# Performance work log

Measured on AMD Instinct MI355X. Metric: run time of the kernel, lower is better.

Reference implementation:

```python
import jax, jax.numpy as jnp
import numpy as np

D_MODEL = 1024; D_STATE = 64; HEADDIM = 64; EXPAND = 2
D_INNER = EXPAND * D_MODEL            # 2048
NHEADS = D_INNER // HEADDIM           # 32
NGROUPS = 1
GN = NGROUPS * D_STATE                # 64
CONV_DIM = D_INNER + 2 * (2 * GN)     # 2304
D_IN_PROJ = 2 * D_INNER + 2 * (2 * GN) + 2 * NHEADS  # 4416
K_SP = 7; K_TP = 4; CHUNK = 256
BATCH = 2; FRAMES = 8; SPATIAL = 256; SEQLEN = SPATIAL * FRAMES  # 2048


def silu(x):
    return x * jax.nn.sigmoid(x)


def flip_frames(x, f):
    # 'b (l f) d -> b l f d' flip frame axis, flatten back
    b, L, d = x.shape
    return x.reshape(b, L // f, f, d)[:, :, ::-1, :].reshape(b, L, d)


def depthwise_conv1d(x, w, b, pad):
    # x: (N, L, C), w: (C, K) depthwise, pad=(lo,hi) -> (N, L_out, C)
    y = jax.lax.conv_general_dilated(
        jnp.transpose(x, (0, 2, 1)), w[:, None, :], (1,), [pad],
        feature_group_count=w.shape[0])
    return jnp.transpose(y + b[None, :, None], (0, 2, 1))


def setup_inputs():
    rng = np.random.default_rng(0)
    f32 = lambda *s: jnp.asarray(rng.standard_normal(s), jnp.float32)
    # dt_bias init exactly as in the torch module
    dt = np.exp(rng.random(NHEADS) * (np.log(0.1) - np.log(0.001)) + np.log(0.001))
    dt = np.clip(dt, 1e-4, None)
    inv_dt = dt + np.log(-np.expm1(-dt))
    return {
        "u": f32(BATCH, SEQLEN, D_MODEL),
        "in_proj_w": f32(D_IN_PROJ, D_MODEL) * 0.02,
        "conv_sp_w": f32(CONV_DIM, K_SP) * 0.2,
        "conv_sp_b": f32(CONV_DIM) * 0.02,
        "conv_tp_w": f32(CONV_DIM, K_TP) * 0.2,
        "conv_tp_b": f32(CONV_DIM) * 0.02,
        "dt_bias": jnp.asarray(inv_dt, jnp.float32),
        "A_log": jnp.zeros((NHEADS,), jnp.float32),
        "D": jnp.ones((NHEADS,), jnp.float32),
        "fc_D_w": f32(NHEADS, D_INNER) * 0.02,
        "norm_w": jnp.ones((D_INNER,), jnp.float32),
        "out_proj_w": f32(D_MODEL, D_INNER) * 0.02,
        "num_frames": FRAMES,
    }


def chunked_scan(xh, dt, A, Bm, Cm, sp, cs):
    # xh:(R,L,h,p) dt:(R,L,h) Bm,Cm:(R,L,n). ngroups=1.
    # seq_idx semantics: rows [0:b) one segment; rows [b:2b) reset every sp tokens.
    R, L, H, P = xh.shape
    nch = L // cs
    b = R // 2
    xch = xh.reshape(R, nch, cs, H, P)
    dtc = jnp.transpose(dt.reshape(R, nch, cs, H), (0, 1, 3, 2))   # (R,nch,h,cs)
    Bch = Bm.reshape(R, nch, cs, D_STATE)
    Cch = Cm.reshape(R, nch, cs, D_STATE)
    a = dtc * A[None, None, :, None]                               # negative logs
    cum = jnp.cumsum(a, axis=-1)                                   # inclusive
    mask = jnp.tril(jnp.ones((cs, cs), bool))
    seg = cum[..., :, None] - cum[..., None, :]                    # (R,nch,h,t,s)
    Lmat = jnp.where(mask, jnp.exp(jnp.where(mask, seg, 0.0)), 0.0)
    CB = jnp.einsum('rctn,rcsn->rcts', Cch, Bch)
    M = CB[:, :, None] * Lmat * dtc[:, :, :, None, :]
    Y_intra = jnp.einsum('rchts,rcshp->rcthp', M, xch)
    # chunk-final states and cross-chunk recurrence
    G = jnp.exp(cum[..., -1:] - cum) * dtc                         # (R,nch,h,cs)
    S_chunk = jnp.einsum('rchs,rcshp,rcsn->rchpn', G, xch, Bch)
    chunk_decay = jnp.exp(cum[..., -1])                            # (R,nch,h)
    cidx = jnp.arange(nch)
    rb = (cidx > 0) & ((cidx * cs) % sp == 0)
    resetc = jnp.concatenate([jnp.zeros((b, nch), bool),
                              jnp.broadcast_to(rb, (b, nch))], axis=0)

    def cstep(S, inp):
        dec, Sc, r = inp
        S = jnp.where(r[:, None, None, None], 0.0, S)
        prev = S
        S = dec[:, :, None, None] * S + Sc
        return S, prev

    S0 = jnp.zeros((R, H, P, D_STATE), xh.dtype)
    _, prevs = jax.lax.scan(
        cstep, S0,
        (jnp.transpose(chunk_decay, (1, 0, 2)),
         jnp.transpose(S_chunk, (1, 0, 2, 3, 4)),
         resetc.T))
    prev_states = jnp.transpose(prevs, (1, 0, 2, 3, 4))            # (R,nch,h,p,n)
    Y_inter = jnp.einsum('rcht,rctn,rchpn->rcthp', jnp.exp(cum), Cch, prev_states)
    return (Y_intra + Y_inter).reshape(R, L, H, P)


def reference(u, in_proj_w, conv_sp_w, conv_sp_b, conv_tp_w, conv_tp_b,
              dt_bias, A_log, D, fc_D_w, norm_w, out_proj_w, num_frames):
    batch, seqlen, _ = u.shape
    f = num_frames
    sp = seqlen // f
    zxbcdt = u @ in_proj_w.T
    z = zxbcdt[..., :D_INNER]
    xBC = zxbcdt[..., D_INNER:D_INNER + CONV_DIM]
    dt_raw = zxbcdt[..., D_INNER + CONV_DIM:]
    dt = jnp.concatenate([dt_raw[..., :NHEADS],
                          flip_frames(dt_raw[..., NHEADS:], f)], axis=0)
    dt = jax.nn.softplus(dt + dt_bias)                             # (2b,L,h)
    A = -jnp.exp(A_log)
    # spatial depthwise conv over spatial dim per frame ('same' pad) + SiLU
    xBC = xBC.reshape(batch, sp, f, CONV_DIM).transpose(0, 2, 1, 3).reshape(batch * f, sp, CONV_DIM)
    xBC = silu(depthwise_conv1d(xBC, conv_sp_w, conv_sp_b, (K_SP // 2, K_SP // 2)))
    # causal temporal depthwise conv over frame dim per spatial location + SiLU
    xBC = xBC.reshape(batch, f, sp, CONV_DIM).transpose(0, 2, 1, 3).reshape(batch * sp, f, CONV_DIM)
    xBC = silu(depthwise_conv1d(xBC, conv_tp_w, conv_tp_b, (K_TP - 1, 0)))
    xBC = xBC.reshape(batch, seqlen, CONV_DIM)
    x = xBC[..., :D_INNER]
    BC = xBC[..., D_INNER:]
    x_orig = x
    x2 = jnp.concatenate([x, flip_frames(x, f)], axis=0)
    BC2 = jnp.concatenate([BC[..., :2 * GN], flip_frames(BC[..., 2 * GN:], f)], axis=0)
    Bm, Cm = BC2[..., :GN], BC2[..., GN:]
    xh = x2.reshape(2 * batch, seqlen, NHEADS, HEADDIM)
    y = chunked_scan(xh, dt, A, Bm, Cm, sp, CHUNK)                 # (2b,L,h,p)
    y_fwd = y[:batch].reshape(batch, seqlen, D_INNER)
    y_rev = y[batch:].reshape(batch, sp, f, D_INNER)
    # roll-by-one with zeroed first position (fwd: token axis, rev: spatial axis)
    y_fwd = jnp.concatenate([jnp.zeros_like(y_fwd[:, :1]), y_fwd[:, :-1]], axis=1)
    y_rev = jnp.concatenate([jnp.zeros_like(y_rev[:, :1]), y_rev[:, :-1]], axis=1)
    y_rev = y_rev[:, :, ::-1, :].reshape(batch, seqlen, D_INNER)
    x_res = x_orig * jnp.repeat(x_orig @ fc_D_w.T + D, HEADDIM, axis=-1)
    y = y_fwd + y_rev + x_res
    # gated RMSNorm (norm_before_gate=True): rmsnorm(y)*w*silu(z)
    y = y * jax.lax.rsqrt(jnp.mean(jnp.square(y), axis=-1, keepdims=True) + 1e-5)
    y = y * norm_w * silu(z)
    return y @ out_proj_w.T
```

## Files before the change

### kernel.cpp

```cpp
#include <hip/hip_runtime.h>
#include <hip/hip_bf16.h>
#include <math.h>

#define D_STATE   64
#define HEADDIM   64
#define D_INNER   2048
#define NHEADS    32
#define GN        64
#define CONV_DIM  2304
#define D_IN_PROJ 4416
#define ZLD       4352
#define K_SP      7
#define K_TP      4
#define CHUNK     256
#define BATCHN    2
#define FRAMES    8
#define SPATIAL   256
#define SEQLEN    2048
#define NCH       8
#define MTOT      4096

typedef __attribute__((ext_vector_type(8))) short short8;
typedef __attribute__((ext_vector_type(8))) unsigned short ushort8v;
typedef __attribute__((ext_vector_type(4))) float floatx4;

__device__ __forceinline__ float silu_f(float x) { return x / (1.f + __expf(-x)); }
__device__ __forceinline__ int flip_l(int l) { return (l & ~7) | (7 - (l & 7)); }
__device__ __forceinline__ unsigned short f2bf(float f) {
  unsigned int u = __float_as_uint(f);
  unsigned int r = (u + 0x7fffu + ((u >> 16) & 1u)) >> 16;
  return (unsigned short)r;
}
__device__ __forceinline__ float bf2f(unsigned short s) {
  return __uint_as_float(((unsigned int)s) << 16);
}
__device__ __forceinline__ unsigned int cvtpk_bf16(float lo, float hi) {
  unsigned int r;
  asm("v_cvt_pk_bf16_f32 %0, %1, %2" : "=v"(r) : "v"(lo), "v"(hi));
  return r;
}
typedef union { short8 v; unsigned int u[4]; } s8u;
__device__ __forceinline__ void gload_lds16(const unsigned short* g, unsigned short* l) {
  __builtin_amdgcn_global_load_lds((const __attribute__((address_space(1))) void*)g,
                                   (__attribute__((address_space(3))) void*)l, 16, 0, 0);
}

__global__ __launch_bounds__(256) void cast3_bf16_kernel(const float* __restrict__ a,
                                                         unsigned short* __restrict__ oa,
                                                         int na,
                                                         const float* __restrict__ b,
                                                         unsigned short* __restrict__ ob,
                                                         int nb,
                                                         const float* __restrict__ c,
                                                         unsigned short* __restrict__ oc) {
  int bid = blockIdx.x;
  const float* in;
  unsigned short* out;
  size_t blk;
  if (bid < na)            { in = a; out = oa; blk = bid; }
  else if (bid < na + nb)  { in = b; out = ob; blk = bid - na; }
  else                     { in = c; out = oc; blk = bid - na - nb; }
  size_t i = (blk * 256 + threadIdx.x) * 4;
  float4 v = *(const float4*)(in + i);
  ushort4 o;
  o.x = f2bf(v.x); o.y = f2bf(v.y); o.z = f2bf(v.z); o.w = f2bf(v.w);
  *(ushort4*)(out + i) = o;
}

__global__ __launch_bounds__(256) void gemm_bk64_bf16out(
    const unsigned short* __restrict__ A, int lda,
    const unsigned short* __restrict__ B, int ldb,
    unsigned short* __restrict__ C, int ldc, int K) {
  __shared__ unsigned short As[128 * 64];
  __shared__ unsigned short Bs[128 * 64];
  const int tid = threadIdx.x;
  const int lane = tid & 63;
  const int w = tid >> 6;
  const int m0 = blockIdx.y * 128;
  const int n0 = blockIdx.x * 128;
  const int wm = (w >> 1) * 64;
  const int wn = (w & 1) * 64;
  const int lrow = lane >> 3;
  const int lperm = lane & 7;
  floatx4 acc[4][4] = {};
  for (int k0 = 0; k0 < K; k0 += 64) {
#pragma unroll
    for (int j = 0; j < 8; ++j) {
      int g = j * 4 + w;
      if (g < 16) {
        int row = g * 8 + lrow;
        int cg = (lperm ^ (row & 7)) * 8;
        gload_lds16(A + (size_t)(m0 + row) * lda + k0 + cg, &As[g * 512]);
      } else {
        int gb = g - 16;
        int row = gb * 8 + lrow;
        int cg = (lperm ^ (row & 7)) * 8;
        gload_lds16(B + (size_t)(n0 + row) * ldb + k0 + cg, &Bs[gb * 512]);
      }
    }
    __syncthreads();
    const int fr = lane & 15;
    const int kq = (lane >> 4) * 8;
#pragma unroll
    for (int kk = 0; kk < 64; kk += 32) {
      int u = (kk + kq) >> 3;
      short8 af[4], bfr[4];
#pragma unroll
      for (int i = 0; i < 4; ++i) {
        int row = wm + i * 16 + fr;
        af[i] = *(const short8*)&As[(row * 8 + (u ^ (row & 7))) * 8];
      }
#pragma unroll
      for (int j = 0; j < 4; ++j) {
        int row = wn + j * 16 + fr;
        bfr[j] = *(const short8*)&Bs[(row * 8 + (u ^ (row & 7))) * 8];
      }
#pragma unroll
      for (int i = 0; i < 4; ++i)
#pragma unroll
        for (int j = 0; j < 4; ++j)
          acc[i][j] = __builtin_amdgcn_mfma_f32_16x16x32_bf16(af[i], bfr[j], acc[i][j], 0, 0, 0);
    }
    __syncthreads();
  }
  const int fr = lane & 15;
  const int rg = (lane >> 4) * 4;
  unsigned short* Ew = &As[w * 1024];
  const int rr = lane >> 3;
  const int c8 = (lane & 7) * 8;
#pragma unroll
  for (int i = 0; i < 4; ++i) {
#pragma unroll
    for (int q = 0; q < 4; ++q)
#pragma unroll
      for (int j = 0; j < 4; ++j)
        Ew[(rg + q) * 64 + j * 16 + fr] = f2bf(acc[i][j][q]);
    ushort8v v0 = *(const ushort8v*)&Ew[rr * 64 + c8];
    ushort8v v1 = *(const ushort8v*)&Ew[(rr + 8) * 64 + c8];
    *(ushort8v*)(C + (size_t)(m0 + wm + i * 16 + rr) * ldc + n0 + wn + c8) = v0;
    *(ushort8v*)(C + (size_t)(m0 + wm + i * 16 + rr + 8) * ldc + n0 + wn + c8) = v1;
  }
}

__global__ __launch_bounds__(256) void gemm_m64_f32(
    const unsigned short* __restrict__ A, int lda,
    const unsigned short* __restrict__ B, int ldb,
    float* __restrict__ C, int ldc, int K) {
  __shared__ unsigned short As[64 * 64];
  __shared__ unsigned short Bs[128 * 64];
  const int tid = threadIdx.x;
  const int lane = tid & 63;
  const int w = tid >> 6;
  const int m0 = blockIdx.y * 64;
  const int n0 = blockIdx.x * 128;
  const int wm = (w >> 1) * 32;
  const int wn = (w & 1) * 64;
  const int lrow = lane >> 3;
  const int lperm = lane & 7;
  floatx4 acc[2][4] = {};
  for (int k0 = 0; k0 < K; k0 += 64) {
#pragma unroll
    for (int j = 0; j < 6; ++j) {
      int g = j * 4 + w;
      if (g < 8) {
        int row = g * 8 + lrow;
        int cg = (lperm ^ (row & 7)) * 8;
        gload_lds16(A + (size_t)(m0 + row) * lda + k0 + cg, &As[g * 512]);
      } else {
        int gb = g - 8;
        int row = gb * 8 + lrow;
        int cg = (lperm ^ (row & 7)) * 8;
        gload_lds16(B + (size_t)(n0 + row) * ldb + k0 + cg, &Bs[gb * 512]);
      }
    }
    __syncthreads();
    const int fr = lane & 15;
    const int kq = (lane >> 4) * 8;
#pragma unroll
    for (int kk = 0; kk < 64; kk += 32) {
      int u = (kk + kq) >> 3;
      short8 af[2], bfr[4];
#pragma unroll
      for (int i = 0; i < 2; ++i) {
        int row = wm + i * 16 + fr;
        af[i] = *(const short8*)&As[(row * 8 + (u ^ (row & 7))) * 8];
      }
#pragma unroll
      for (int j = 0; j < 4; ++j) {
        int row = wn + j * 16 + fr;
        bfr[j] = *(const short8*)&Bs[(row * 8 + (u ^ (row & 7))) * 8];
      }
#pragma unroll
      for (int i = 0; i < 2; ++i)
#pragma unroll
        for (int j = 0; j < 4; ++j)
          acc[i][j] = __builtin_amdgcn_mfma_f32_16x16x32_bf16(af[i], bfr[j], acc[i][j], 0, 0, 0);
    }
    __syncthreads();
  }
  const int col = lane & 15;
  const int rg = (lane >> 4) * 4;
#pragma unroll
  for (int i = 0; i < 2; ++i)
#pragma unroll
    for (int j = 0; j < 4; ++j)
#pragma unroll
      for (int r = 0; r < 4; ++r)
        C[(size_t)(m0 + wm + i * 16 + rg + r) * ldc + (n0 + wn + j * 16 + col)] = acc[i][j][r];
}

__global__ __launch_bounds__(256) void gemm_ts_mfma(
    const unsigned short* __restrict__ A, int lda,
    const float* __restrict__ B, int ldb,
    float* __restrict__ C, int ldc, int N, int K) {
  __shared__ float red[4][1024];
  const int tid = threadIdx.x;
  const int lane = tid & 63;
  const int w = tid >> 6;
  const int m0 = blockIdx.x * 16;
  const int fr = lane & 15;
  const int kq = (lane >> 4) * 8;
  const int nt = N >> 4;
  const int kseg = K >> 2;
  const int k0 = w * kseg;
  floatx4 acc[4] = {};
  for (int k = k0; k < k0 + kseg; k += 32) {
    short8 af = *(const short8*)(A + (size_t)(m0 + fr) * lda + k + kq);
    for (int j = 0; j < nt; ++j) {
      const float* bp = B + (size_t)(j * 16 + fr) * ldb + k + kq;
      float4 b0 = *(const float4*)bp;
      float4 b1 = *(const float4*)(bp + 4);
      short8 bf8;
      bf8[0] = (short)f2bf(b0.x); bf8[1] = (short)f2bf(b0.y);
      bf8[2] = (short)f2bf(b0.z); bf8[3] = (short)f2bf(b0.w);
      bf8[4] = (short)f2bf(b1.x); bf8[5] = (short)f2bf(b1.y);
      bf8[6] = (short)f2bf(b1.z); bf8[7] = (short)f2bf(b1.w);
      acc[j] = __builtin_amdgcn_mfma_f32_16x16x32_bf16(af, bf8, acc[j], 0, 0, 0);
    }
  }
  const int rg = (lane >> 4) * 4;
  for (int j = 0; j < nt; ++j)
#pragma unroll
    for (int q = 0; q < 4; ++q)
      red[w][j * 256 + (rg + q) * 16 + fr] = acc[j][q];
  __syncthreads();
  const int entries = nt * 256;
  for (int e = tid; e < entries; e += 256) {
    float s = red[0][e] + red[1][e] + red[2][e] + red[3][e];
    int j = e >> 8, idx = e & 255, row = idx >> 4, col = idx & 15;
    C[(size_t)(m0 + row) * ldc + j * 16 + col] = s;
  }
}

__global__ __launch_bounds__(256) void dtscan_kernel(const float* __restrict__ DTraw,
                                                     const float* __restrict__ dt_bias,
                                                     const float* __restrict__ A_log,
                                                     float* __restrict__ DTt,
                                                     float* __restrict__ CUMS) {
  __shared__ float sc[256];
  int tid = threadIdx.x;
  int idx = blockIdx.x * 256 + tid;
  int l  = idx & 2047;
  int rh = idx >> 11;
  int h  = rh & 31;
  int r  = rh >> 5;
  int bi = r & 1;
  int ls = (r < 2) ? l : flip_l(l);
  int ch = (r < 2) ? h : NHEADS + h;
  float raw = DTraw[((size_t)bi * SEQLEN + ls) * 64 + ch] + dt_bias[h];
  float dtv = (raw > 20.f) ? raw : log1pf(__expf(raw));
  DTt[idx] = dtv;
  float A = -__expf(A_log[h]);
  float run = dtv * A;
  sc[tid] = run;
  __syncthreads();
#pragma unroll
  for (int ofs = 1; ofs < 256; ofs <<= 1) {
    float add = (tid >= ofs) ? sc[tid - ofs] : 0.f;
    __syncthreads();
    run += add;
    sc[tid] = run;
    __syncthreads();
  }
  CUMS[idx] = run;
}

__global__ __launch_bounds__(256) void conv_fused2_kernel(const unsigned short* __restrict__ Zb,
                                                          const float* __restrict__ wsp,
                                                          const float* __restrict__ bsp,
                                                          const float* __restrict__ wtp,
                                                          const float* __restrict__ btp,
                                                          unsigned short* __restrict__ XTb) {
  __shared__ float4 xsl[8][8][32];
  const int tid = threadIdx.x;
  const int g  = tid & 31;
  const int fr = tid >> 5;
  const int c  = blockIdx.x * 128 + g * 4;
  const int s0 = blockIdx.y * 8;
  const int bi = blockIdx.z;
  float wsp_r[4][K_SP];
#pragma unroll
  for (int ch = 0; ch < 4; ++ch)
#pragma unroll
    for (int j = 0; j < K_SP; ++j) wsp_r[ch][j] = wsp[(c + ch) * K_SP + j];
  float4 bsp4 = *(const float4*)(bsp + c);
  float4 z[14];
#pragma unroll
  for (int i = 0; i < 14; ++i) {
    int ss = s0 - 3 + i;
    if (0 <= ss && ss < SPATIAL) {
      ushort4 v = *(const ushort4*)(Zb + ((size_t)bi * SEQLEN + (ss*8 + fr)) * ZLD + D_INNER + c);
      z[i] = make_float4(bf2f(v.x), bf2f(v.y), bf2f(v.z), bf2f(v.w));
    } else {
      z[i] = make_float4(0.f, 0.f, 0.f, 0.f);
    }
  }
#pragma unroll
  for (int so = 0; so < 8; ++so) {
    float4 a = bsp4;
#pragma unroll
    for (int j = 0; j < K_SP; ++j) {
      a.x += wsp_r[0][j] * z[so + j].x;
      a.y += wsp_r[1][j] * z[so + j].y;
      a.z += wsp_r[2][j] * z[so + j].z;
      a.w += wsp_r[3][j] * z[so + j].w;
    }
    a.x = silu_f(a.x); a.y = silu_f(a.y); a.z = silu_f(a.z); a.w = silu_f(a.w);
    xsl[fr][so][g] = a;
  }
  __syncthreads();
  float wtp_r[4][K_TP];
#pragma unroll
  for (int ch = 0; ch < 4; ++ch)
#pragma unroll
    for (int j = 0; j < K_TP; ++j) wtp_r[ch][j] = wtp[(c + ch) * K_TP + j];
  float4 btp4 = *(const float4*)(btp + c);
#pragma unroll
  for (int so = 0; so < 8; ++so) {
    float4 t = btp4;
#pragma unroll
    for (int j = 0; j < K_TP; ++j) {
      int ff = fr + j - (K_TP - 1);
      if (ff >= 0) {
        float4 xv = xsl[ff][so][g];
        t.x += wtp_r[0][j] * xv.x;
        t.y += wtp_r[1][j] * xv.y;
        t.z += wtp_r[2][j] * xv.z;
        t.w += wtp_r[3][j] * xv.w;
      }
    }
    ushort4 o;
    o.x = f2bf(silu_f(t.x)); o.y = f2bf(silu_f(t.y));
    o.z = f2bf(silu_f(t.z)); o.w = f2bf(silu_f(t.w));
    *(ushort4*)(XTb + ((size_t)bi * SEQLEN + ((s0 + so)*8 + fr)) * CONV_DIM + c) = o;
  }
}

__global__ __launch_bounds__(256) void cb_kernel(const unsigned short* __restrict__ XTb,
                                                 float* __restrict__ CBs) {
  __shared__ float Ct[64][65];
  __shared__ float Bt[64][65];
  int tid = threadIdx.x;
  int t0 = (blockIdx.x & 3) * 64;
  int s0 = (blockIdx.x >> 2) * 64;
  if (s0 > t0) return;
  int c = blockIdx.y;
  int r = blockIdx.z;
  int bi = r & 1;
  int bOff = D_INNER + ((r < 2) ? 0 : 2*GN);
  int cOff = bOff + GN;
  int lrow = tid >> 4;
  int n4 = (tid & 15) << 2;
#pragma unroll
  for (int rep = 0; rep < 4; ++rep) {
    int tl = rep * 16 + lrow;
    int Lc = c * CHUNK + t0 + tl;
    int Ls = c * CHUNK + s0 + tl;
    if (r >= 2) { Lc = flip_l(Lc); Ls = flip_l(Ls); }
    ushort4 cv = *(const ushort4*)(XTb + ((size_t)bi*SEQLEN + Lc)*CONV_DIM + cOff + n4);
    ushort4 bv = *(const ushort4*)(XTb + ((size_t)bi*SEQLEN + Ls)*CONV_DIM + bOff + n4);
    Ct[n4+0][tl] = bf2f(cv.x); Ct[n4+1][tl] = bf2f(cv.y);
    Ct[n4+2][tl] = bf2f(cv.z); Ct[n4+3][tl] = bf2f(cv.w);
    Bt[n4+0][tl] = bf2f(bv.x); Bt[n4+1][tl] = bf2f(bv.y);
    Bt[n4+2][tl] = bf2f(bv.z); Bt[n4+3][tl] = bf2f(bv.w);
  }
  __syncthreads();
  int txx = tid & 15;
  int tyy = tid >> 4;
  float acc[4][4] = {{0.f,0.f,0.f,0.f},{0.f,0.f,0.f,0.f},{0.f,0.f,0.f,0.f},{0.f,0.f,0.f,0.f}};
#pragma unroll
  for (int n = 0; n < D_STATE; ++n) {
    float cr[4], br[4];
#pragma unroll
    for (int i = 0; i < 4; ++i) cr[i] = Ct[n][tyy + 16*i];
#pragma unroll
    for (int j = 0; j < 4; ++j) br[j] = Bt[n][txx + 16*j];
#pragma unroll
    for (int i = 0; i < 4; ++i)
#pragma unroll
      for (int j = 0; j < 4; ++j)
        acc[i][j] += cr[i] * br[j];
  }
  size_t base = (((size_t)r*NCH + c) * CHUNK) * CHUNK;
#pragma unroll
  for (int i = 0; i < 4; ++i)
#pragma unroll
    for (int j = 0; j < 4; ++j)
      CBs[base + (size_t)(t0 + tyy + 16*i)*CHUNK + (s0 + txx + 16*j)] = acc[i][j];
}

__global__ __launch_bounds__(256) void chunk_state_kernel(const unsigned short* __restrict__ XTb,
                                                          const float* __restrict__ DTt,
                                                          const float* __restrict__ CUMS,
                                                          float* __restrict__ SCH) {
  __shared__ unsigned short Xs[64 * 136];
  __shared__ unsigned short Bs[64 * 136];
  __shared__ float gs[CHUNK];
  int tid = threadIdx.x;
  int lane = tid & 63;
  int w = tid >> 6;
  int c = blockIdx.x;
  int h = blockIdx.y;
  int r = blockIdx.z;
  int bi = r;
  int rh = r * NHEADS + h;
  float cl = CUMS[(size_t)rh*SEQLEN + c*CHUNK + 255];
  gs[tid] = __expf(cl - CUMS[(size_t)rh*SEQLEN + c*CHUNK + tid]) * DTt[(size_t)rh*SEQLEN + c*CHUNK + tid];
  const int fr = lane & 15;
  const int kq = (lane >> 4) * 8;
  const int sr = tid >> 3;
  const int p0 = (tid & 7) * 8;
  const int swz = (tid & 7) << 3;
  floatx4 acc[4] = {};
  for (int half = 0; half < 2; ++half) {
    __syncthreads();
#pragma unroll
    for (int P = 0; P < 4; ++P) {
      int s = P * 32 + sr;
      int l = c*CHUNK + half*128 + s;
      const unsigned short* row = XTb + ((size_t)bi*SEQLEN + l)*CONV_DIM;
      ushort8v xv = *(const ushort8v*)(row + h*HEADDIM + p0);
      ushort8v bv = *(const ushort8v*)(row + D_INNER + p0);
      float g = gs[half*128 + s];
      int cswz = s ^ swz;
#pragma unroll
      for (int q = 0; q < 8; ++q) {
        Xs[(p0 + q) * 136 + cswz] = f2bf(g * bf2f(xv[q]));
        Bs[(p0 + q) * 136 + cswz] = bv[q];
      }
    }
    __syncthreads();
#pragma unroll
    for (int sl = 0; sl < 4; ++sl) {
      int s0 = sl * 32;
      int Ra = w*16 + fr;
      short8 af = *(const short8*)&Xs[Ra * 136 + ((s0 + kq) ^ (((Ra >> 3) & 7) << 3))];
#pragma unroll
      for (int j = 0; j < 4; ++j) {
        int Rb = j*16 + fr;
        short8 bf8 = *(const short8*)&Bs[Rb * 136 + ((s0 + kq) ^ (((Rb >> 3) & 7) << 3))];
        acc[j] = __builtin_amdgcn_mfma_f32_16x16x32_bf16(af, bf8, acc[j], 0, 0, 0);
      }
    }
  }
  const int col = lane & 15;
  const int rg = (lane >> 4) * 4;
  size_t base = (((size_t)r*NCH + c)*NHEADS + h) * (size_t)(HEADDIM*D_STATE);
#pragma unroll
  for (int j = 0; j < 4; ++j)
#pragma unroll
    for (int q = 0; q < 4; ++q)
      SCH[base + (size_t)(w*16 + rg + q)*D_STATE + j*16 + col] = acc[j][q];
}

__global__ __launch_bounds__(256) void state_combine_kernel(const float* __restrict__ SCH,
                                                            const float* __restrict__ CUMS,
                                                            float* __restrict__ SPREV) {
  int bid = blockIdx.x;
  int pq = bid & 3;
  int h = (bid >> 2) & 31;
  int r = bid >> 7;
  int tid = threadIdx.x;
  int p = pq*16 + (tid >> 4);
  int n = (tid & 15) * 4;
  float4 S = make_float4(0.f, 0.f, 0.f, 0.f);
  for (int c = 0; c < NCH; ++c) {
    size_t off = ((((size_t)r*NCH + c)*NHEADS + h)*HEADDIM + p)*D_STATE + n;
    *(float4*)(SPREV + off) = S;
    float dec = __expf(CUMS[((size_t)r*NHEADS + h)*SEQLEN + c*CHUNK + 255]);
    float4 v = *(const float4*)(SCH + off);
    S.x = dec*S.x + v.x; S.y = dec*S.y + v.y;
    S.z = dec*S.z + v.z; S.w = dec*S.w + v.w;
  }
}

#define YS_ED(S0)                                                              \
  float edv[8];                                                                \
  { float4 e0_ = *(const float4*)&ecd[(S0) + kq];                              \
    float4 e1_ = *(const float4*)&ecd[(S0) + kq + 4];                          \
    edv[0]=e0_.x; edv[1]=e0_.y; edv[2]=e0_.z; edv[3]=e0_.w;                    \
    edv[4]=e1_.x; edv[5]=e1_.y; edv[6]=e1_.z; edv[7]=e1_.w; }

#define YS_BFR(S0)                                                             \
  short8 bfr[4];                                                               \
  _Pragma("unroll")                                                            \
  for (int j = 0; j < 4; ++j) {                                                \
    int R = j * 16 + fr;                                                       \
    bfr[j] = *(const short8*)&Xt[R * 264 + (((S0) + kq) ^ (((R >> 3) & 7) << 3))]; \
  }

#define YS_MFMA4(AF, ACCROW)                                                   \
  _Pragma("unroll")                                                            \
  for (int j = 0; j < 4; ++j)                                                  \
    ACCROW[j] = __builtin_amdgcn_mfma_f32_16x16x32_bf16(AF, bfr[j], ACCROW[j], 0, 0, 0);

#define YS_AF_NOMASK(C0, C1, E)                                                \
  { af_.u[0] = cvtpk_bf16(C0.x*(E)*edv[0], C0.y*(E)*edv[1]);                   \
    af_.u[1] = cvtpk_bf16(C0.z*(E)*edv[2], C0.w*(E)*edv[3]);                   \
    af_.u[2] = cvtpk_bf16(C1.x*(E)*edv[4], C1.y*(E)*edv[5]);                   \
    af_.u[3] = cvtpk_bf16(C1.z*(E)*edv[6], C1.w*(E)*edv[7]); }

#define YS_AF_MASK(C0, C1, E, TROW)                                            \
  { float wz[8] = {C0.x,C0.y,C0.z,C0.w,C1.x,C1.y,C1.z,C1.w};                   \
    _Pragma("unroll")                                                          \
    for (int jj = 0; jj < 8; ++jj) {                                           \
      float t_ = wz[jj]*(E)*edv[jj];                                           \
      wz[jj] = (kq + jj <= (TROW)) ? t_ : 0.f; }                               \
    af_.u[0]=cvtpk_bf16(wz[0],wz[1]); af_.u[1]=cvtpk_bf16(wz[2],wz[3]);        \
    af_.u[2]=cvtpk_bf16(wz[4],wz[5]); af_.u[3]=cvtpk_bf16(wz[6],wz[7]); }

#define YS_STRIP(KS, E2, ACC)                                                  \
  {                                                                            \
    const int t0s_ = (KS) * 32;                                                \
    const float* cbr0 = CBs + cbbase + (size_t)(t0s_ + fr) * CHUNK + kq;       \
    const float* cbr1 = cbr0 + (size_t)16 * CHUNK;                             \
    float4 a0 = *(const float4*)cbr0;                                          \
    float4 a1 = *(const float4*)(cbr0 + 4);                                    \
    float4 b0 = *(const float4*)cbr1;                                          \
    float4 b1 = *(const float4*)(cbr1 + 4);                                    \
    for (int sl = 0; sl < (KS); ++sl) {                                        \
      int s0 = sl * 32;                                                        \
      float4 na0 = *(const float4*)(cbr0 + s0 + 32);                           \
      float4 na1 = *(const float4*)(cbr0 + s0 + 36);                           \
      float4 nb0 = *(const float4*)(cbr1 + s0 + 32);                           \
      float4 nb1 = *(const float4*)(cbr1 + s0 + 36);                           \
      YS_ED(s0); YS_BFR(s0);                                                   \
      s8u af_;                                                                 \
      YS_AF_NOMASK(a0, a1, (E2)[0]);                                           \
      YS_MFMA4(af_.v, ACC[0]);                                                 \
      YS_AF_NOMASK(b0, b1, (E2)[1]);                                           \
      YS_MFMA4(af_.v, ACC[1]);                                                 \
      a0 = na0; a1 = na1; b0 = nb0; b1 = nb1;                                  \
    }                                                                          \
    {                                                                          \
      int s0 = (KS) * 32;                                                      \
      YS_ED(s0); YS_BFR(s0);                                                   \
      s8u af_;                                                                 \
      YS_AF_MASK(a0, a1, (E2)[0], fr);                                         \
      YS_MFMA4(af_.v, ACC[0]);                                                 \
      YS_AF_MASK(b0, b1, (E2)[1], 16 + fr);                                    \
      YS_MFMA4(af_.v, ACC[1]);                                                 \
    }                                                                          \
  }

#define YS_INTER(T0S, E2, ACC)                                                 \
  _Pragma("unroll")                                                            \
  for (int i = 0; i < 2; ++i) {                                                \
    int t = (T0S) + i * 16 + fr;                                               \
    const unsigned short* crow = XTb + ((size_t)bi*SEQLEN + c*CHUNK + t)*CONV_DIM + D_INNER + GN + n0 + kq; \
    ushort4 c0 = *(const ushort4*)crow;                                        \
    ushort4 c1 = *(const ushort4*)(crow + 4);                                  \
    float eI = (E2)[i];                                                        \
    s8u af_;                                                                   \
    af_.u[0] = cvtpk_bf16(bf2f(c0.x)*eI, bf2f(c0.y)*eI);                       \
    af_.u[1] = cvtpk_bf16(bf2f(c0.z)*eI, bf2f(c0.w)*eI);                       \
    af_.u[2] = cvtpk_bf16(bf2f(c1.x)*eI, bf2f(c1.y)*eI);                       \
    af_.u[3] = cvtpk_bf16(bf2f(c1.z)*eI, bf2f(c1.w)*eI);                       \
    YS_MFMA4(af_.v, ACC[i]);                                                   \
  }

#define YS_EPI(T0S, ACC)                                                       \
  _Pragma("unroll")                                                            \
  for (int i = 0; i < 2; ++i) {                                                \
    _Pragma("unroll")                                                          \
    for (int q = 0; q < 4; ++q)                                                \
      _Pragma("unroll")                                                        \
      for (int j = 0; j < 4; ++j)                                              \
        Ew[(rg + q) * 64 + j * 16 + fr] = f2bf(ACC[i][j][q]);                  \
    ushort8v v0 = *(const ushort8v*)&Ew[rr * 64 + c8];                         \
    ushort8v v1 = *(const ushort8v*)&Ew[(rr + 8) * 64 + c8];                   \
    *(ushort8v*)(Yb16 + ybase + (size_t)((T0S) + i*16 + rr) * D_INNER + c8) = v0;      \
    *(ushort8v*)(Yb16 + ybase + (size_t)((T0S) + i*16 + rr + 8) * D_INNER + c8) = v1;  \
  }

__global__ __launch_bounds__(256, 4) void yscan_kernel(const unsigned short* __restrict__ XTb,
                                                       const float* __restrict__ DTt,
                                                       const float* __restrict__ CUMS,
                                                       const float* __restrict__ CBs,
                                                       const float* __restrict__ SPREV,
                                                       unsigned short* __restrict__ Yb16) {
  __shared__ unsigned short Xt[64 * 264];
  __shared__ float cums[CHUNK];
  __shared__ float ecd[CHUNK];
  int tid = threadIdx.x;
  int lane = tid & 63;
  int w = tid >> 6;
  int id = blockIdx.x;
  int c = id & 7;
  int h = (id >> 3) & 31;
  int r = id >> 8;
  int rh = r * NHEADS + h;
  int bi = r & 1;
  {
    int sr = tid >> 3;
    int p0 = (tid & 7) * 8;
    int swz = (tid & 7) << 3;
#pragma unroll
    for (int P = 0; P < 8; ++P) {
      int s = P * 32 + sr;
      int L = c * CHUNK + s;
      if (r >= 2) L = flip_l(L);
      ushort8v v = *(const ushort8v*)(XTb + ((size_t)bi * SEQLEN + L) * CONV_DIM + h * HEADDIM + p0);
      int cswz = s ^ swz;
#pragma unroll
      for (int q = 0; q < 8; ++q)
        Xt[(p0 + q) * 264 + cswz] = v[q];
    }
    float cv = CUMS[(size_t)rh * SEQLEN + c * CHUNK + tid];
    cums[tid] = cv;
    ecd[tid] = __expf(-cv) * DTt[(size_t)rh * SEQLEN + c * CHUNK + tid];
  }
  __syncthreads();
  const int fr = lane & 15;
  const int kq = (lane >> 4) * 8;
  const int kA = w, kB = 7 - w;
  const int tA = kA * 32, tB = kB * 32;
  float eAr[2], eBr[2];
#pragma unroll
  for (int i = 0; i < 2; ++i) {
    eAr[i] = __expf(cums[tA + i * 16 + fr]);
    eBr[i] = __expf(cums[tB + i * 16 + fr]);
  }
  floatx4 accA[2][4] = {};
  floatx4 accB[2][4] = {};
  size_t cbbase = (((size_t)r * NCH + c) * CHUNK) * CHUNK;
  YS_STRIP(kA, eAr, accA);
  YS_STRIP(kB, eBr, accB);
  if (r < 2) {
    const float* spbase = SPREV + (((size_t)r*NCH + c)*NHEADS + h) * (size_t)(HEADDIM*D_STATE);
#pragma unroll
    for (int ns = 0; ns < 2; ++ns) {
      int n0 = ns * 32;
      short8 bfr[4];
#pragma unroll
      for (int j = 0; j < 4; ++j) {
        const float* sp = spbase + (size_t)(j*16 + fr)*D_STATE + n0 + kq;
        float4 s0v = *(const float4*)sp;
        float4 s1v = *(const float4*)(sp + 4);
        s8u bb;
        bb.u[0] = cvtpk_bf16(s0v.x, s0v.y);
        bb.u[1] = cvtpk_bf16(s0v.z, s0v.w);
        bb.u[2] = cvtpk_bf16(s1v.x, s1v.y);
        bb.u[3] = cvtpk_bf16(s1v.z, s1v.w);
        bfr[j] = bb.v;
      }
      YS_INTER(tA, eAr, accA);
      YS_INTER(tB, eBr, accB);
    }
  }
  __syncthreads();
  unsigned short* Ew = Xt + w * 1024;
  const int rg = (lane >> 4) * 4;
  const int rr = lane >> 3;
  const int c8 = (lane & 7) * 8;
  size_t ybase = ((size_t)r*SEQLEN + c*CHUNK)*D_INNER + h*HEADDIM;
  YS_EPI(tA, accA);
  YS_EPI(tB, accB);
}

__global__ __launch_bounds__(256) void combine_kernel(const unsigned short* __restrict__ Y,
                                                      const unsigned short* __restrict__ XTb,
                                                      const float* __restrict__ FCD,
                                                      const float* __restrict__ Dp,
                                                      const unsigned short* __restrict__ Zb,
                                                      const float* __restrict__ norm_w,
                                                      unsigned short* __restrict__ YPb) {
  __shared__ float red[256];
  int row = blockIdx.x;
  int bi = row >> 11;
  int l = row & 2047;
  int s = l >> 3, fr = l & 7;
  int tid = threadIdx.x;
  int d0 = tid * 8;
  const unsigned short* yf = (l >= 1) ? Y + ((size_t)bi*SEQLEN + (l-1))*D_INNER + d0 : nullptr;
  const unsigned short* yr = (s >= 1) ? Y + ((size_t)(2+bi)*SEQLEN + ((s-1)*8 + (7-fr)))*D_INNER + d0 : nullptr;
  const unsigned short* xr = XTb + ((size_t)row)*CONV_DIM + d0;
  float fcv = FCD[(size_t)row*NHEADS + (d0 >> 6)] + Dp[d0 >> 6];
  ushort8v xv8 = *(const ushort8v*)xr;
  float v[8];
#pragma unroll
  for (int q = 0; q < 8; ++q) v[q] = bf2f(xv8[q]) * fcv;
  if (yf) {
    ushort8v a = *(const ushort8v*)yf;
#pragma unroll
    for (int q = 0; q < 8; ++q) v[q] += bf2f(a[q]);
  }
  if (yr) {
    ushort8v a = *(const ushort8v*)yr;
#pragma unroll
    for (int q = 0; q < 8; ++q) v[q] += bf2f(a[q]);
  }
  float ss = 0.f;
#pragma unroll
  for (int q = 0; q < 8; ++q) ss += v[q] * v[q];
  red[tid] = ss;
  __syncthreads();
  for (int ofs = 128; ofs > 0; ofs >>= 1) {
    if (tid < ofs) red[tid] += red[tid + ofs];
    __syncthreads();
  }
  float rs = rsqrtf(red[0] / (float)D_INNER + 1e-5f);
  ushort8v zv8 = *(const ushort8v*)(Zb + ((size_t)row)*ZLD + d0);
  float4 nw0 = *(const float4*)(norm_w + d0);
  float4 nw1 = *(const float4*)(norm_w + d0 + 4);
  float nw[8] = {nw0.x,nw0.y,nw0.z,nw0.w,nw1.x,nw1.y,nw1.z,nw1.w};
  ushort8v o;
#pragma unroll
  for (int q = 0; q < 8; ++q)
    o[q] = f2bf(v[q] * rs * nw[q] * silu_f(bf2f(zv8[q])));
  *(ushort8v*)(YPb + (size_t)row*D_INNER + d0) = o;
}

extern "C" void kernel_launch(void* const* d_in, const int* in_sizes, int n_in,
                              void* d_out, int out_size, void* d_ws, size_t ws_size,
                              hipStream_t stream) {
  (void)in_sizes; (void)n_in; (void)out_size; (void)ws_size;
  const float* u          = (const float*)d_in[0];
  const float* in_proj_w  = (const float*)d_in[1];
  const float* conv_sp_w  = (const float*)d_in[2];
  const float* conv_sp_b  = (const float*)d_in[3];
  const float* conv_tp_w  = (const float*)d_in[4];
  const float* conv_tp_b  = (const float*)d_in[5];
  const float* dt_bias    = (const float*)d_in[6];
  const float* A_log      = (const float*)d_in[7];
  const float* Dp         = (const float*)d_in[8];
  const float* fc_D_w     = (const float*)d_in[9];
  const float* norm_w     = (const float*)d_in[10];
  const float* out_proj_w = (const float*)d_in[11];
  float* out = (float*)d_out;
  float* ws = (float*)d_ws;

  float* Z     = ws;
  float* SH    = Z     + 17825792ULL;
  float* XT    = SH    + 9437184ULL;
  float* DTt   = XT    + 9437184ULL;
  float* Yb    = DTt   + 262144ULL;
  float* SPREV = Yb    + 16777216ULL;
  float* FCD   = SPREV + 2097152ULL;
  float* DTraw = FCD   + 131072ULL;
  float* CUMS  = DTraw + 262144ULL;

  unsigned short* Zb   = (unsigned short*)Z;
  unsigned short* XTb  = (unsigned short*)XT;
  unsigned short* Yb16 = (unsigned short*)Yb;
  unsigned short* Ub   = (unsigned short*)Yb;
  unsigned short* Wb   = (unsigned short*)Yb + 4194304ULL;
  float* SCH = Yb + 8388608ULL;
  unsigned short* Wob = (unsigned short*)(Yb + 10485760ULL);
  unsigned short* YPb = (unsigned short*)SH;

  cast3_bf16_kernel<<<10496, 256, 0, stream>>>(u, Ub, 4096, in_proj_w, Wb, 4352,
                                               out_proj_w, Wob);
  gemm_bk64_bf16out<<<dim3(34, 32), 256, 0, stream>>>(Ub, 1024, Wb, 1024, Zb, ZLD, 1024);
  gemm_ts_mfma<<<256, 256, 0, stream>>>(Ub, 1024, in_proj_w + 4352ULL*1024, 1024,
                                        DTraw, 64, 64, 1024);
  dtscan_kernel<<<1024, 256, 0, stream>>>(DTraw, dt_bias, A_log, DTt, CUMS);
  conv_fused2_kernel<<<dim3(18, 32, 2), 256, 0, stream>>>(Zb, conv_sp_w, conv_sp_b,
                                                          conv_tp_w, conv_tp_b, XTb);
  gemm_ts_mfma<<<256, 256, 0, stream>>>(XTb, CONV_DIM, fc_D_w, 2048,
                                        FCD, 32, 32, 2048);
  cb_kernel<<<dim3(16, 8, 4), 256, 0, stream>>>(XTb, SH);
  chunk_state_kernel<<<dim3(NCH, NHEADS, 2), 256, 0, stream>>>(XTb, DTt, CUMS, SCH);
  state_combine_kernel<<<256, 256, 0, stream>>>(SCH, CUMS, SPREV);
  yscan_kernel<<<dim3(1024), 256, 0, stream>>>(XTb, DTt, CUMS, SH, SPREV, Yb16);
  combine_kernel<<<4096, 256, 0, stream>>>(Yb16, XTb, FCD, Dp, Zb, norm_w, YPb);
  gemm_m64_f32<<<dim3(8, 64), 256, 0, stream>>>(YPb, 2048, Wob, 2048, out, 1024, 2048);
}
```

Measured before the change: 328.7 us.

## Remap GEMM blocks per XCD, use MFMA in cb_kernel, shuffle-reduce RMS norm

The two GEMMs switch to a 1D grid whose block index is remapped so each XCD (bid&7) handles a contiguous rectangular region of output tiles, improving L2 reuse of A and B tiles. cb_kernel drops its LDS-staged FP32 outer-product loop in favour of bf16 MFMA 16x16x32 instructions that read fragments directly from global memory. combine_kernel replaces its shared-memory tree reduction, which synchronised at every step, with wave shuffles plus a single four-element LDS reduction. The MFMA path accumulates from bf16 inputs in fp32, as the FP32 version already did after converting from bf16, so numerics should stay close.

```diff
diff --git a/kernel.cpp b/kernel.cpp
--- a/kernel.cpp
+++ b/kernel.cpp
@@ -76,8 +76,13 @@
   const int tid = threadIdx.x;
   const int lane = tid & 63;
   const int w = tid >> 6;
-  const int m0 = blockIdx.y * 128;
-  const int n0 = blockIdx.x * 128;
+  const int bid = blockIdx.x;
+  const int xcd = bid & 7;
+  const int rp  = bid >> 3;
+  const int px  = rp % 17;
+  const int py  = rp / 17;
+  const int m0 = ((xcd >> 1) * 8 + py) * 128;
+  const int n0 = ((xcd & 1) * 17 + px) * 128;
   const int wm = (w >> 1) * 64;
   const int wn = (w & 1) * 64;
   const int lrow = lane >> 3;
@@ -151,8 +156,14 @@
   const int tid = threadIdx.x;
   const int lane = tid & 63;
   const int w = tid >> 6;
-  const int m0 = blockIdx.y * 64;
-  const int n0 = blockIdx.x * 128;
+  const int bid = blockIdx.x;
+  const int xcd = bid & 7;
+  const int q8  = bid >> 3;
+  const int rsel = q8 >> 5;
+  const int rp   = q8 & 31;
+  const int reg  = xcd + 8 * rsel;
+  const int m0 = ((reg >> 1) * 8 + (rp >> 2)) * 64;
+  const int n0 = ((reg & 1) * 4 + (rp & 3)) * 128;
   const int wm = (w >> 1) * 32;
   const int wn = (w & 1) * 64;
   const int lrow = lane >> 3;
@@ -358,9 +369,9 @@
 
 __global__ __launch_bounds__(256) void cb_kernel(const unsigned short* __restrict__ XTb,
                                                  float* __restrict__ CBs) {
-  __shared__ float Ct[64][65];
-  __shared__ float Bt[64][65];
   int tid = threadIdx.x;
+  int lane = tid & 63;
+  int w = tid >> 6;
   int t0 = (blockIdx.x & 3) * 64;
   int s0 = (blockIdx.x >> 2) * 64;
   if (s0 > t0) return;
@@ -369,44 +380,32 @@
   int bi = r & 1;
   int bOff = D_INNER + ((r < 2) ? 0 : 2*GN);
   int cOff = bOff + GN;
-  int lrow = tid >> 4;
-  int n4 = (tid & 15) << 2;
-#pragma unroll
-  for (int rep = 0; rep < 4; ++rep) {
-    int tl = rep * 16 + lrow;
-    int Lc = c * CHUNK + t0 + tl;
-    int Ls = c * CHUNK + s0 + tl;
-    if (r >= 2) { Lc = flip_l(Lc); Ls = flip_l(Ls); }
-    ushort4 cv = *(const ushort4*)(XTb + ((size_t)bi*SEQLEN + Lc)*CONV_DIM + cOff + n4);
-    ushort4 bv = *(const ushort4*)(XTb + ((size_t)bi*SEQLEN + Ls)*CONV_DIM + bOff + n4);
-    Ct[n4+0][tl] = bf2f(cv.x); Ct[n4+1][tl] = bf2f(cv.y);
-    Ct[n4+2][tl] = bf2f(cv.z); Ct[n4+3][tl] = bf2f(cv.w);
-    Bt[n4+0][tl] = bf2f(bv.x); Bt[n4+1][tl] = bf2f(bv.y);
-    Bt[n4+2][tl] = bf2f(bv.z); Bt[n4+3][tl] = bf2f(bv.w);
-  }
-  __syncthreads();
-  int txx = tid & 15;
-  int tyy = tid >> 4;
-  float acc[4][4] = {{0.f,0.f,0.f,0.f},{0.f,0.f,0.f,0.f},{0.f,0.f,0.f,0.f},{0.f,0.f,0.f,0.f}};
-#pragma unroll
-  for (int n = 0; n < D_STATE; ++n) {
-    float cr[4], br[4];
-#pragma unroll
-    for (int i = 0; i < 4; ++i) cr[i] = Ct[n][tyy + 16*i];
-#pragma unroll
-    for (int j = 0; j < 4; ++j) br[j] = Bt[n][txx + 16*j];
-#pragma unroll
-    for (int i = 0; i < 4; ++i)
-#pragma unroll
-      for (int j = 0; j < 4; ++j)
-        acc[i][j] += cr[i] * br[j];
-  }
+  const int fr = lane & 15;
+  const int kq = (lane >> 4) * 8;
+  int Lc = c * CHUNK + t0 + w * 16 + fr;
+  if (r >= 2) Lc = flip_l(Lc);
+  const unsigned short* crow = XTb + ((size_t)bi*SEQLEN + Lc)*CONV_DIM + cOff;
+  short8 af0 = *(const short8*)(crow + kq);
+  short8 af1 = *(const short8*)(crow + 32 + kq);
+  floatx4 acc[4] = {};
+#pragma unroll
+  for (int j = 0; j < 4; ++j) {
+    int Ls = c * CHUNK + s0 + j * 16 + fr;
+    if (r >= 2) Ls = flip_l(Ls);
+    const unsigned short* brow = XTb + ((size_t)bi*SEQLEN + Ls)*CONV_DIM + bOff;
+    short8 bf0 = *(const short8*)(brow + kq);
+    short8 bf1 = *(const short8*)(brow + 32 + kq);
+    acc[j] = __builtin_amdgcn_mfma_f32_16x16x32_bf16(af0, bf0, acc[j], 0, 0, 0);
+    acc[j] = __builtin_amdgcn_mfma_f32_16x16x32_bf16(af1, bf1, acc[j], 0, 0, 0);
+  }
+  const int col = lane & 15;
+  const int rg = (lane >> 4) * 4;
   size_t base = (((size_t)r*NCH + c) * CHUNK) * CHUNK;
 #pragma unroll
-  for (int i = 0; i < 4; ++i)
-#pragma unroll
-    for (int j = 0; j < 4; ++j)
-      CBs[base + (size_t)(t0 + tyy + 16*i)*CHUNK + (s0 + txx + 16*j)] = acc[i][j];
+  for (int j = 0; j < 4; ++j)
+#pragma unroll
+    for (int q = 0; q < 4; ++q)
+      CBs[base + (size_t)(t0 + w*16 + rg + q)*CHUNK + (s0 + j*16 + col)] = acc[j][q];
 }
 
 __global__ __launch_bounds__(256) void chunk_state_kernel(const unsigned short* __restrict__ XTb,
@@ -685,7 +684,7 @@
                                                       const unsigned short* __restrict__ Zb,
                                                       const float* __restrict__ norm_w,
                                                       unsigned short* __restrict__ YPb) {
-  __shared__ float red[256];
+  __shared__ float red4[4];
   int row = blockIdx.x;
   int bi = row >> 11;
   int l = row & 2047;
@@ -713,13 +712,12 @@
   float ss = 0.f;
 #pragma unroll
   for (int q = 0; q < 8; ++q) ss += v[q] * v[q];
-  red[tid] = ss;
+#pragma unroll
+  for (int d = 1; d < 64; d <<= 1) ss += __shfl_xor(ss, d, 64);
+  if ((tid & 63) == 0) red4[tid >> 6] = ss;
   __syncthreads();
-  for (int ofs = 128; ofs > 0; ofs >>= 1) {
-    if (tid < ofs) red[tid] += red[tid + ofs];
-    __syncthreads();
-  }
-  float rs = rsqrtf(red[0] / (float)D_INNER + 1e-5f);
+  float tot = red4[0] + red4[1] + red4[2] + red4[3];
+  float rs = rsqrtf(tot / (float)D_INNER + 1e-5f);
   ushort8v zv8 = *(const ushort8v*)(Zb + ((size_t)row)*ZLD + d0);
   float4 nw0 = *(const float4*)(norm_w + d0);
   float4 nw1 = *(const float4*)(norm_w + d0 + 4);
@@ -771,7 +769,7 @@
 
   cast3_bf16_kernel<<<10496, 256, 0, stream>>>(u, Ub, 4096, in_proj_w, Wb, 4352,
                                                out_proj_w, Wob);
-  gemm_bk64_bf16out<<<dim3(34, 32), 256, 0, stream>>>(Ub, 1024, Wb, 1024, Zb, ZLD, 1024);
+  gemm_bk64_bf16out<<<dim3(1088), 256, 0, stream>>>(Ub, 1024, Wb, 1024, Zb, ZLD, 1024);
   gemm_ts_mfma<<<256, 256, 0, stream>>>(Ub, 1024, in_proj_w + 4352ULL*1024, 1024,
                                         DTraw, 64, 64, 1024);
   dtscan_kernel<<<1024, 256, 0, stream>>>(DTraw, dt_bias, A_log, DTt, CUMS);
@@ -784,5 +782,5 @@
   state_combine_kernel<<<256, 256, 0, stream>>>(SCH, CUMS, SPREV);
   yscan_kernel<<<dim3(1024), 256, 0, stream>>>(XTb, DTt, CUMS, SH, SPREV, Yb16);
   combine_kernel<<<4096, 256, 0, stream>>>(Yb16, XTb, FCD, Dp, Zb, norm_w, YPb);
-  gemm_m64_f32<<<dim3(8, 64), 256, 0, stream>>>(YPb, 2048, Wob, 2048, out, 1024, 2048);
-}
+  gemm_m64_f32<<<dim3(512), 256, 0, stream>>>(YPb, 2048, Wob, 2048, out, 1024, 2048);
+}
```

After: 321.8 us. 1.02x faster.
